# Kernel tuning notes

Measured on AMD Instinct MI355X. Metric: run time of the kernel, lower is better.

Reference implementation:

```python
import jax, jax.numpy as jnp
import numpy as np

B, N, E = 2, 2048, 1024
H, D = 16, 64  # context_dim = H*D = 1024


def setup_inputs() -> dict:
    key = jax.random.key(0)
    ks = jax.random.split(key, 6)
    s = 0.02
    return {
        "input_emb": jax.random.normal(ks[0], (B, N, E), dtype=jnp.float32),
        "Wq": jax.random.normal(ks[1], (E, H * D), dtype=jnp.float32) * s,
        "Wk": jax.random.normal(ks[2], (E, D), dtype=jnp.float32) * s,
        "Wv": jax.random.normal(ks[3], (E, D), dtype=jnp.float32) * s,
        "Wo": jax.random.normal(ks[4], (H * D, H * D), dtype=jnp.float32) * s,
        "bo": jax.random.normal(ks[5], (H * D,), dtype=jnp.float32) * s,
    }


def reference(input_emb, Wq, Wk, Wv, Wo, bo):
    b, n, _ = input_emb.shape
    Q = (input_emb @ Wq).reshape(b, n, H, D)          # (B,N,H,D)
    K = input_emb @ Wk                                 # (B,N,D) shared across heads (MQA)
    V = input_emb @ Wv                                 # (B,N,D)
    # scores: (B,H,N,N); mask is applied before scaling in the torch code,
    # but -inf/scale == -inf so mask-then-scale == scale-then-mask.
    scores = jnp.einsum("bnhd,bmd->bhnm", Q, K) / jnp.sqrt(jnp.float32(D))
    causal = jnp.tril(jnp.ones((n, n), dtype=bool))    # True = keep
    scores = jnp.where(causal[None, None], scores, -jnp.inf)
    weights = jax.nn.softmax(scores, axis=-1)          # dropout rate 0.0 -> identity
    Z = jnp.einsum("bhnm,bmd->bnhd", weights, V).reshape(b, n, H * D)
    return Z @ Wo + bo
```

## Files before the change

### kernel.cpp

```cpp
#include <hip/hip_runtime.h>
#include <hip/hip_bf16.h>


#define NQ 2048
#define BATCH 2
#define HEADS 16
#define HD 64
#define EMB 1024
#define NKV 1152

typedef short s16x8 __attribute__((ext_vector_type(8)));
typedef float f32x4 __attribute__((ext_vector_type(4)));
typedef unsigned short ushort_t;

__device__ __forceinline__ ushort_t f2bf(float f) {
    unsigned u = __builtin_bit_cast(unsigned, f);
    u += 0x7fff + ((u >> 16) & 1);
    return (ushort_t)(u >> 16);
}

__device__ __forceinline__ void store_out(float* p, float v) { *p = v; }
__device__ __forceinline__ void store_out(ushort_t* p, float v) { *p = f2bf(v); }

#define GL16(g, l)                                                                  \
    __builtin_amdgcn_global_load_lds(                                               \
        (const __attribute__((address_space(1))) unsigned int*)(g),                 \
        (__attribute__((address_space(3))) unsigned int*)(l), 16, 0, 0)

__global__ __launch_bounds__(256) void prep(const float* __restrict__ x,
                                            const float* __restrict__ Wq,
                                            const float* __restrict__ Wk,
                                            const float* __restrict__ Wv,
                                            const float* __restrict__ Wo,
                                            ushort_t* __restrict__ xb,
                                            ushort_t* __restrict__ Wqkv_t,
                                            ushort_t* __restrict__ Wo_t) {
    const int bid = blockIdx.x, t = threadIdx.x;
    if (bid < 4096) {
        const int i = bid * 1024 + t * 4;
        const float4 v = *(const float4*)&x[i];
        ushort_t o[4] = {f2bf(v.x), f2bf(v.y), f2bf(v.z), f2bf(v.w)};
        *(uint2*)&xb[i] = *(uint2*)o;
        return;
    }
    int tb = bid - 4096;
    const float* src; ushort_t* dst; int N, n0, k0;
    if (tb < 1024)      { src = Wq; N = 1024; dst = Wqkv_t;
                          n0 = (tb & 31) * 32; k0 = (tb >> 5) * 32; }
    else if (tb < 1088) { tb -= 1024; src = Wk; N = 64; dst = Wqkv_t + (size_t)1024 * EMB;
                          n0 = (tb & 1) * 32; k0 = (tb >> 1) * 32; }
    else if (tb < 1152) { tb -= 1088; src = Wv; N = 64; dst = Wqkv_t + (size_t)1088 * EMB;
                          n0 = (tb & 1) * 32; k0 = (tb >> 1) * 32; }
    else                { tb -= 1152; src = Wo; N = 1024; dst = Wo_t;
                          n0 = (tb & 31) * 32; k0 = (tb >> 5) * 32; }
    __shared__ float tile[32][33];
    const int tx = t & 31, ty = t >> 5;
#pragma unroll
    for (int i = 0; i < 32; i += 8)
        tile[ty + i][tx] = src[(size_t)(k0 + ty + i) * N + n0 + tx];
    __syncthreads();
#pragma unroll
    for (int i = 0; i < 32; i += 8)
        dst[(size_t)(n0 + ty + i) * EMB + k0 + tx] = f2bf(tile[tx][ty + i]);
}

template<bool HAS_BIAS, bool WRITE_VT, typename OutT>
__global__ __launch_bounds__(256) void gemm_bf16(const ushort_t* __restrict__ A,
                                                 const ushort_t* __restrict__ Bt,
                                                 const float* __restrict__ bias,
                                                 OutT* __restrict__ C,
                                                 ushort_t* __restrict__ Vt,
                                                 int M, int N, int K) {
    __shared__ __align__(16) ushort_t Al[64 * 32];
    __shared__ __align__(16) ushort_t Bl[128 * 32];
    const int t = threadIdx.x;
    const int w = t >> 6, lane = t & 63, quad = lane >> 4, ln = lane & 15;
    const int row0 = blockIdx.y * 64, col0 = blockIdx.x * 128;

    const int rA = t >> 2;
    const int lcA = (t & 3) ^ ((rA >> 1) & 3);
    const int rB1 = 64 + rA;
    const ushort_t* ga  = A  + (size_t)(row0 + rA) * K + lcA * 8;
    const ushort_t* gb0 = Bt + (size_t)(col0 + rA) * K + lcA * 8;
    const ushort_t* gb1 = Bt + (size_t)(col0 + rB1) * K + lcA * 8;
    ushort_t* lA  = Al + w * 512;
    ushort_t* lB0 = Bl + w * 512;
    ushort_t* lB1 = Bl + 2048 + w * 512;

    f32x4 acc[4][2] = {};
    const int sw = (ln >> 1) & 3;
    for (int k0 = 0; k0 < K; k0 += 32) {
        GL16(ga, lA); GL16(gb0, lB0); GL16(gb1, lB1);
        ga += 32; gb0 += 32; gb1 += 32;
        __syncthreads();

        s16x8 af[4], bf[2];
#pragma unroll
        for (int mt = 0; mt < 4; ++mt)
            af[mt] = *(const s16x8*)&Al[(mt * 16 + ln) * 32 + ((quad ^ sw) * 8)];
#pragma unroll
        for (int nt = 0; nt < 2; ++nt)
            bf[nt] = *(const s16x8*)&Bl[(w * 32 + nt * 16 + ln) * 32 + ((quad ^ sw) * 8)];
#pragma unroll
        for (int mt = 0; mt < 4; ++mt)
#pragma unroll
            for (int nt = 0; nt < 2; ++nt)
                acc[mt][nt] = __builtin_amdgcn_mfma_f32_16x16x32_bf16(
                    af[mt], bf[nt], acc[mt][nt], 0, 0, 0);
        __syncthreads();
    }

#pragma unroll
    for (int nt = 0; nt < 2; ++nt) {
        const int col = col0 + w * 32 + nt * 16 + ln;
        const float bv = HAS_BIAS ? bias[col] : 0.f;
#pragma unroll
        for (int mt = 0; mt < 4; ++mt) {
#pragma unroll
            for (int r = 0; r < 4; ++r) {
                const int row = row0 + mt * 16 + quad * 4 + r;
                store_out(&C[(size_t)row * N + col], acc[mt][nt][r] + bv);
            }
            if (WRITE_VT && col >= 1088) {
                const int d = col - 1088;
                const int n = row0 + mt * 16 + quad * 4;
                const int bb = n >> 11, nn = n & 2047;
                ushort_t tmp[4] = {f2bf(acc[mt][nt][0]), f2bf(acc[mt][nt][1]),
                                   f2bf(acc[mt][nt][2]), f2bf(acc[mt][nt][3])};
                *(uint2*)&Vt[((size_t)bb * 64 + d) * NQ + nn] = *(uint2*)tmp;
            }
        }
    }
}

__device__ __forceinline__ void stage_tile(ushort_t* lds, const ushort_t* g,
                                           size_t rstride, int w, int lane) {
#pragma unroll
    for (int it = 0; it < 2; ++it) {
        const int u = (w * 2 + it) * 64 + lane;
        const int row = u >> 3, pc = u & 7;
        const int lc = pc ^ (row & 7);
        GL16(g + (size_t)row * rstride + lc * 8, lds + (size_t)(w * 2 + it) * 512);
    }
}

__device__ __forceinline__ s16x8 frag(const ushort_t* lds, int row, int lc) {
    const int phys = lc ^ (row & 7);
    return *(const s16x8*)&lds[row * 64 + phys * 8];
}

__global__ __launch_bounds__(256, 4) void attn_mfma(const ushort_t* __restrict__ QKV,
                                                    const ushort_t* __restrict__ Vt,
                                                    ushort_t* __restrict__ Z) {
    const int bid = blockIdx.x;
    const int b = (bid >> 4) & 1, h = bid & 15;
    const int i = bid >> 5, k = i >> 3, j = i & 7;
    const int qt = (k == 0) ? 2 * j : (k == 1) ? 31 - 2 * j
                 : (k == 2) ? 2 * j + 1 : 30 - 2 * j;
    const int t = threadIdx.x;
    const int w = t >> 6, lane = t & 63, quad = lane >> 4, ln = lane & 15;

    __shared__ __align__(16) ushort_t QPs[64 * 64];
    __shared__ __align__(16) ushort_t Kl[2][64 * 64];
    __shared__ __align__(16) ushort_t Vl[2][64 * 64];

    const ushort_t* Kg = QKV + (size_t)b * NQ * NKV + 1024;
    const ushort_t* Vg = Vt + (size_t)b * 64 * NQ;

    stage_tile(QPs, QKV + (size_t)(b * NQ + qt * 64) * NKV + h * HD, NKV, w, lane);
    stage_tile(Kl[0], Kg, NKV, w, lane);
    stage_tile(Vl[0], Vg, NQ, w, lane);
    __syncthreads();

    const s16x8 aQ0 = frag(QPs, w * 16 + ln, quad);
    const s16x8 aQ1 = frag(QPs, w * 16 + ln, 4 + quad);

    f32x4 o[4];
#pragma unroll
    for (int ii = 0; ii < 4; ++ii) o[ii] = f32x4{0.f, 0.f, 0.f, 0.f};
    float mrow[4], lrow[4];
#pragma unroll
    for (int r = 0; r < 4; ++r) { mrow[r] = -1e30f; lrow[r] = 0.f; }

#pragma unroll 1
    for (int jt = 0; jt <= qt; ++jt) {
        const int cur = jt & 1;
        if (jt < qt) {
            stage_tile(Kl[cur ^ 1], Kg + (size_t)(jt + 1) * 64 * NKV, NKV, w, lane);
            stage_tile(Vl[cur ^ 1], Vg + (jt + 1) * 64, NQ, w, lane);
        }
        const ushort_t* Kc = Kl[cur];
        const ushort_t* Vc = Vl[cur];

        f32x4 s[4];
#pragma unroll
        for (int nt = 0; nt < 4; ++nt) {
            f32x4 acc = f32x4{0.f, 0.f, 0.f, 0.f};
            const s16x8 b0 = frag(Kc, nt * 16 + ln, quad);
            const s16x8 b1 = frag(Kc, nt * 16 + ln, 4 + quad);
            acc = __builtin_amdgcn_mfma_f32_16x16x32_bf16(aQ0, b0, acc, 0, 0, 0);
            acc = __builtin_amdgcn_mfma_f32_16x16x32_bf16(aQ1, b1, acc, 0, 0, 0);
            s[nt] = acc;
        }

        const bool diag = (jt == qt);
        float rmax[4];
#pragma unroll
        for (int r = 0; r < 4; ++r) rmax[r] = -1e30f;
#pragma unroll
        for (int nt = 0; nt < 4; ++nt)
#pragma unroll
            for (int r = 0; r < 4; ++r) {
                float v = s[nt][r] * 0.125f;
                if (diag && (nt * 16 + ln) > (w * 16 + quad * 4 + r)) v = -1e30f;
                s[nt][r] = v;
                rmax[r] = fmaxf(rmax[r], v);
            }
#pragma unroll
        for (int r = 0; r < 4; ++r) {
            rmax[r] = fmaxf(rmax[r], __shfl_xor(rmax[r], 1));
            rmax[r] = fmaxf(rmax[r], __shfl_xor(rmax[r], 2));
            rmax[r] = fmaxf(rmax[r], __shfl_xor(rmax[r], 4));
            rmax[r] = fmaxf(rmax[r], __shfl_xor(rmax[r], 8));
        }
        float alpha[4], rsum[4];
#pragma unroll
        for (int r = 0; r < 4; ++r) {
            const float mnew = fmaxf(mrow[r], rmax[r]);
            alpha[r] = __expf(mrow[r] - mnew);
            mrow[r] = mnew;
            rsum[r] = 0.f;
        }
#pragma unroll
        for (int nt = 0; nt < 4; ++nt)
#pragma unroll
            for (int r = 0; r < 4; ++r) {
                const float pv = __expf(s[nt][r] - mrow[r]);
                s[nt][r] = pv;
                rsum[r] += pv;
            }
#pragma unroll
        for (int r = 0; r < 4; ++r) {
            rsum[r] += __shfl_xor(rsum[r], 1);
            rsum[r] += __shfl_xor(rsum[r], 2);
            rsum[r] += __shfl_xor(rsum[r], 4);
            rsum[r] += __shfl_xor(rsum[r], 8);
            lrow[r] = lrow[r] * alpha[r] + rsum[r];
        }
#pragma unroll
        for (int ntd = 0; ntd < 4; ++ntd)
#pragma unroll
            for (int r = 0; r < 4; ++r) o[ntd][r] *= alpha[r];

#pragma unroll
        for (int nt = 0; nt < 4; ++nt)
#pragma unroll
            for (int r = 0; r < 4; ++r) {
                const int prow = quad * 4 + r;
                const int pc = (nt * 2 + (ln >> 3)) ^ (prow & 7);
                QPs[(w * 16 + prow) * 64 + pc * 8 + (ln & 7)] = f2bf(s[nt][r]);
            }
        asm volatile("s_waitcnt lgkmcnt(0)" ::: "memory");

        const s16x8 aP0 = frag(QPs, w * 16 + ln, quad);
        const s16x8 aP1 = frag(QPs, w * 16 + ln, 4 + quad);
#pragma unroll
        for (int ntd = 0; ntd < 4; ++ntd) {
            const s16x8 b0 = frag(Vc, ntd * 16 + ln, quad);
            const s16x8 b1 = frag(Vc, ntd * 16 + ln, 4 + quad);
            o[ntd] = __builtin_amdgcn_mfma_f32_16x16x32_bf16(aP0, b0, o[ntd], 0, 0, 0);
            o[ntd] = __builtin_amdgcn_mfma_f32_16x16x32_bf16(aP1, b1, o[ntd], 0, 0, 0);
        }
        __syncthreads();
    }

    float invl[4];
#pragma unroll
    for (int r = 0; r < 4; ++r) invl[r] = 1.f / lrow[r];
#pragma unroll
    for (int ntd = 0; ntd < 4; ++ntd)
#pragma unroll
        for (int r = 0; r < 4; ++r) {
            const size_t row = (size_t)(b * NQ + qt * 64 + w * 16 + quad * 4 + r);
            Z[row * EMB + h * HD + ntd * 16 + ln] = f2bf(o[ntd][r] * invl[r]);
        }
}

extern "C" void kernel_launch(void* const* d_in, const int* in_sizes, int n_in,
                              void* d_out, int out_size, void* d_ws, size_t ws_size,
                              hipStream_t stream) {
    const float* x  = (const float*)d_in[0];
    const float* Wq = (const float*)d_in[1];
    const float* Wk = (const float*)d_in[2];
    const float* Wv = (const float*)d_in[3];
    const float* Wo = (const float*)d_in[4];
    const float* bo = (const float*)d_in[5];
    float* out = (float*)d_out;

    const int M = BATCH * NQ;
    char* ws = (char*)d_ws;
    ushort_t* xb     = (ushort_t*)ws;
    ushort_t* Wqkv_t = (ushort_t*)(ws + (size_t)8  * 1024 * 1024);
    ushort_t* Wo_t   = (ushort_t*)(ws + (size_t)11 * 1024 * 1024);
    ushort_t* QKV    = (ushort_t*)(ws + (size_t)13 * 1024 * 1024);
    ushort_t* Vt     = (ushort_t*)(ws + (size_t)23 * 1024 * 1024);
    ushort_t* Zb     = (ushort_t*)(ws + (size_t)24 * 1024 * 1024);

    dim3 blk(256);
    prep<<<dim3(6272), blk, 0, stream>>>(x, Wq, Wk, Wv, Wo, xb, Wqkv_t, Wo_t);
    gemm_bf16<false, true, ushort_t><<<dim3(NKV / 128, M / 64), blk, 0, stream>>>(
        xb, Wqkv_t, nullptr, QKV, Vt, M, NKV, EMB);
    attn_mfma<<<dim3(1024), blk, 0, stream>>>(QKV, Vt, Zb);
    gemm_bf16<true, false, float><<<dim3(EMB / 128, M / 64), blk, 0, stream>>>(
        Zb, Wo_t, bo, out, nullptr, M, EMB, EMB);
}
```

Baseline: 188.5 us.

## Transpose attention MFMA layout to keep P in registers, fold scale into Q

The QK^T MFMA now takes K as the A operand, so each lane holds one query row. K rows are permuted during staging so the score fragment can be packed straight into the B operand of the PV MFMA with v_cvt_pk_bf16_f32, removing the LDS round trip for P and the Q staging buffer. The softmax scale and log2(e) are folded into Q in the projection GEMM epilogue so exp2 can be used, and rescaling of the running max is skipped when the max grows by at most 8. It also adds s_setprio around the MFMA blocks and vectorizes the Z stores, at the cost of tricky index permutations that must stay consistent.

```diff
diff --git a/kernel.cpp b/kernel.cpp
--- a/kernel.cpp
+++ b/kernel.cpp
@@ -11,6 +11,7 @@
 
 typedef short s16x8 __attribute__((ext_vector_type(8)));
 typedef float f32x4 __attribute__((ext_vector_type(4)));
+typedef unsigned int u32x4 __attribute__((ext_vector_type(4)));
 typedef unsigned short ushort_t;
 
 __device__ __forceinline__ ushort_t f2bf(float f) {
@@ -119,7 +120,9 @@
 #pragma unroll
             for (int r = 0; r < 4; ++r) {
                 const int row = row0 + mt * 16 + quad * 4 + r;
-                store_out(&C[(size_t)row * N + col], acc[mt][nt][r] + bv);
+                float v = acc[mt][nt][r] + bv;
+                if (WRITE_VT && col < 1024) v *= 0.18033688011112043f;
+                store_out(&C[(size_t)row * N + col], v);
             }
             if (WRITE_VT && col >= 1088) {
                 const int d = col - 1088;
@@ -141,6 +144,19 @@
         const int row = u >> 3, pc = u & 7;
         const int lc = pc ^ (row & 7);
         GL16(g + (size_t)row * rstride + lc * 8, lds + (size_t)(w * 2 + it) * 512);
+    }
+}
+
+__device__ __forceinline__ void stage_k(ushort_t* lds, const ushort_t* g,
+                                        int w, int lane) {
+#pragma unroll
+    for (int it = 0; it < 2; ++it) {
+        const int u = (w * 2 + it) * 64 + lane;
+        const int row = u >> 3, pc = u & 7;
+        const int lc = pc ^ (row & 7);
+        const int grow = (row & 32) | (((row >> 2) & 3) << 3) |
+                         (((row >> 4) & 1) << 2) | (row & 3);
+        GL16(g + (size_t)grow * NKV + lc * 8, lds + (size_t)(w * 2 + it) * 512);
     }
 }
 
@@ -160,130 +176,126 @@
     const int t = threadIdx.x;
     const int w = t >> 6, lane = t & 63, quad = lane >> 4, ln = lane & 15;
 
-    __shared__ __align__(16) ushort_t QPs[64 * 64];
     __shared__ __align__(16) ushort_t Kl[2][64 * 64];
     __shared__ __align__(16) ushort_t Vl[2][64 * 64];
 
     const ushort_t* Kg = QKV + (size_t)b * NQ * NKV + 1024;
     const ushort_t* Vg = Vt + (size_t)b * 64 * NQ;
 
-    stage_tile(QPs, QKV + (size_t)(b * NQ + qt * 64) * NKV + h * HD, NKV, w, lane);
-    stage_tile(Kl[0], Kg, NKV, w, lane);
+    const ushort_t* Qg = QKV + (size_t)(b * NQ + qt * 64 + w * 16 + ln) * NKV + h * HD;
+    const s16x8 aQ0 = *(const s16x8*)(Qg + quad * 8);
+    const s16x8 aQ1 = *(const s16x8*)(Qg + 32 + quad * 8);
+
+    stage_k(Kl[0], Kg, w, lane);
     stage_tile(Vl[0], Vg, NQ, w, lane);
     __syncthreads();
 
-    const s16x8 aQ0 = frag(QPs, w * 16 + ln, quad);
-    const s16x8 aQ1 = frag(QPs, w * 16 + ln, 4 + quad);
-
     f32x4 o[4];
 #pragma unroll
     for (int ii = 0; ii < 4; ++ii) o[ii] = f32x4{0.f, 0.f, 0.f, 0.f};
-    float mrow[4], lrow[4];
-#pragma unroll
-    for (int r = 0; r < 4; ++r) { mrow[r] = -1e30f; lrow[r] = 0.f; }
+    float mrow = -1e30f, lrow = 0.f;
+    const int qrel = w * 16 + ln;
 
 #pragma unroll 1
     for (int jt = 0; jt <= qt; ++jt) {
         const int cur = jt & 1;
         if (jt < qt) {
-            stage_tile(Kl[cur ^ 1], Kg + (size_t)(jt + 1) * 64 * NKV, NKV, w, lane);
+            stage_k(Kl[cur ^ 1], Kg + (size_t)(jt + 1) * 64 * NKV, w, lane);
             stage_tile(Vl[cur ^ 1], Vg + (jt + 1) * 64, NQ, w, lane);
         }
         const ushort_t* Kc = Kl[cur];
         const ushort_t* Vc = Vl[cur];
 
         f32x4 s[4];
+        __builtin_amdgcn_s_setprio(1);
 #pragma unroll
         for (int nt = 0; nt < 4; ++nt) {
             f32x4 acc = f32x4{0.f, 0.f, 0.f, 0.f};
-            const s16x8 b0 = frag(Kc, nt * 16 + ln, quad);
-            const s16x8 b1 = frag(Kc, nt * 16 + ln, 4 + quad);
-            acc = __builtin_amdgcn_mfma_f32_16x16x32_bf16(aQ0, b0, acc, 0, 0, 0);
-            acc = __builtin_amdgcn_mfma_f32_16x16x32_bf16(aQ1, b1, acc, 0, 0, 0);
+            acc = __builtin_amdgcn_mfma_f32_16x16x32_bf16(
+                frag(Kc, nt * 16 + ln, quad), aQ0, acc, 0, 0, 0);
+            acc = __builtin_amdgcn_mfma_f32_16x16x32_bf16(
+                frag(Kc, nt * 16 + ln, 4 + quad), aQ1, acc, 0, 0, 0);
             s[nt] = acc;
         }
-
-        const bool diag = (jt == qt);
-        float rmax[4];
-#pragma unroll
-        for (int r = 0; r < 4; ++r) rmax[r] = -1e30f;
+        __builtin_amdgcn_s_setprio(0);
+
+        if (jt == qt) {
+#pragma unroll
+            for (int nt = 0; nt < 4; ++nt)
+#pragma unroll
+                for (int r = 0; r < 4; ++r) {
+                    const int kv = (nt >> 1) * 32 + quad * 8 + (nt & 1) * 4 + r;
+                    if (kv > qrel) s[nt][r] = -1e30f;
+                }
+        }
+
+        float m0 = fmaxf(fmaxf(s[0][0], s[0][1]), fmaxf(s[0][2], s[0][3]));
+        float m1 = fmaxf(fmaxf(s[1][0], s[1][1]), fmaxf(s[1][2], s[1][3]));
+        float m2 = fmaxf(fmaxf(s[2][0], s[2][1]), fmaxf(s[2][2], s[2][3]));
+        float m3 = fmaxf(fmaxf(s[3][0], s[3][1]), fmaxf(s[3][2], s[3][3]));
+        float rmax = fmaxf(fmaxf(m0, m1), fmaxf(m2, m3));
+        rmax = fmaxf(rmax, __shfl_xor(rmax, 16));
+        rmax = fmaxf(rmax, __shfl_xor(rmax, 32));
+
+        if (!__all(rmax - mrow <= 8.f)) {
+            const float mnew = fmaxf(mrow, rmax);
+            const float al = __builtin_amdgcn_exp2f(mrow - mnew);
+            mrow = mnew;
+            lrow *= al;
+#pragma unroll
+            for (int ntd = 0; ntd < 4; ++ntd)
+#pragma unroll
+                for (int r = 0; r < 4; ++r) o[ntd][r] *= al;
+        }
+
+        float rsum = 0.f;
 #pragma unroll
         for (int nt = 0; nt < 4; ++nt)
 #pragma unroll
             for (int r = 0; r < 4; ++r) {
-                float v = s[nt][r] * 0.125f;
-                if (diag && (nt * 16 + ln) > (w * 16 + quad * 4 + r)) v = -1e30f;
-                s[nt][r] = v;
-                rmax[r] = fmaxf(rmax[r], v);
+                const float pv = __builtin_amdgcn_exp2f(s[nt][r] - mrow);
+                s[nt][r] = pv;
+                rsum += pv;
             }
-#pragma unroll
-        for (int r = 0; r < 4; ++r) {
-            rmax[r] = fmaxf(rmax[r], __shfl_xor(rmax[r], 1));
-            rmax[r] = fmaxf(rmax[r], __shfl_xor(rmax[r], 2));
-            rmax[r] = fmaxf(rmax[r], __shfl_xor(rmax[r], 4));
-            rmax[r] = fmaxf(rmax[r], __shfl_xor(rmax[r], 8));
-        }
-        float alpha[4], rsum[4];
-#pragma unroll
-        for (int r = 0; r < 4; ++r) {
-            const float mnew = fmaxf(mrow[r], rmax[r]);
-            alpha[r] = __expf(mrow[r] - mnew);
-            mrow[r] = mnew;
-            rsum[r] = 0.f;
-        }
-#pragma unroll
-        for (int nt = 0; nt < 4; ++nt)
-#pragma unroll
-            for (int r = 0; r < 4; ++r) {
-                const float pv = __expf(s[nt][r] - mrow[r]);
-                s[nt][r] = pv;
-                rsum[r] += pv;
-            }
-#pragma unroll
-        for (int r = 0; r < 4; ++r) {
-            rsum[r] += __shfl_xor(rsum[r], 1);
-            rsum[r] += __shfl_xor(rsum[r], 2);
-            rsum[r] += __shfl_xor(rsum[r], 4);
-            rsum[r] += __shfl_xor(rsum[r], 8);
-            lrow[r] = lrow[r] * alpha[r] + rsum[r];
-        }
-#pragma unroll
-        for (int ntd = 0; ntd < 4; ++ntd)
-#pragma unroll
-            for (int r = 0; r < 4; ++r) o[ntd][r] *= alpha[r];
-
-#pragma unroll
-        for (int nt = 0; nt < 4; ++nt)
-#pragma unroll
-            for (int r = 0; r < 4; ++r) {
-                const int prow = quad * 4 + r;
-                const int pc = (nt * 2 + (ln >> 3)) ^ (prow & 7);
-                QPs[(w * 16 + prow) * 64 + pc * 8 + (ln & 7)] = f2bf(s[nt][r]);
-            }
-        asm volatile("s_waitcnt lgkmcnt(0)" ::: "memory");
-
-        const s16x8 aP0 = frag(QPs, w * 16 + ln, quad);
-        const s16x8 aP1 = frag(QPs, w * 16 + ln, 4 + quad);
+        rsum += __shfl_xor(rsum, 16);
+        rsum += __shfl_xor(rsum, 32);
+        lrow += rsum;
+
+        unsigned pw0[4], pw1[4];
+#pragma unroll
+        for (int jj = 0; jj < 4; ++jj) {
+            const int nt0 = jj >> 1, rr = 2 * (jj & 1);
+            asm("v_cvt_pk_bf16_f32 %0, %1, %2"
+                : "=v"(pw0[jj]) : "v"(s[nt0][rr]), "v"(s[nt0][rr + 1]));
+            asm("v_cvt_pk_bf16_f32 %0, %1, %2"
+                : "=v"(pw1[jj]) : "v"(s[2 + nt0][rr]), "v"(s[2 + nt0][rr + 1]));
+        }
+        const u32x4 q0 = {pw0[0], pw0[1], pw0[2], pw0[3]};
+        const u32x4 q1 = {pw1[0], pw1[1], pw1[2], pw1[3]};
+        const s16x8 bP0 = __builtin_bit_cast(s16x8, q0);
+        const s16x8 bP1 = __builtin_bit_cast(s16x8, q1);
+
+        __builtin_amdgcn_s_setprio(1);
 #pragma unroll
         for (int ntd = 0; ntd < 4; ++ntd) {
-            const s16x8 b0 = frag(Vc, ntd * 16 + ln, quad);
-            const s16x8 b1 = frag(Vc, ntd * 16 + ln, 4 + quad);
-            o[ntd] = __builtin_amdgcn_mfma_f32_16x16x32_bf16(aP0, b0, o[ntd], 0, 0, 0);
-            o[ntd] = __builtin_amdgcn_mfma_f32_16x16x32_bf16(aP1, b1, o[ntd], 0, 0, 0);
-        }
+            o[ntd] = __builtin_amdgcn_mfma_f32_16x16x32_bf16(
+                frag(Vc, ntd * 16 + ln, quad), bP0, o[ntd], 0, 0, 0);
+            o[ntd] = __builtin_amdgcn_mfma_f32_16x16x32_bf16(
+                frag(Vc, ntd * 16 + ln, 4 + quad), bP1, o[ntd], 0, 0, 0);
+        }
+        __builtin_amdgcn_s_setprio(0);
         __syncthreads();
     }
 
-    float invl[4];
-#pragma unroll
-    for (int r = 0; r < 4; ++r) invl[r] = 1.f / lrow[r];
-#pragma unroll
-    for (int ntd = 0; ntd < 4; ++ntd)
-#pragma unroll
-        for (int r = 0; r < 4; ++r) {
-            const size_t row = (size_t)(b * NQ + qt * 64 + w * 16 + quad * 4 + r);
-            Z[row * EMB + h * HD + ntd * 16 + ln] = f2bf(o[ntd][r] * invl[r]);
-        }
+    const float invl = 1.f / lrow;
+    const size_t row = (size_t)(b * NQ + qt * 64 + w * 16 + ln);
+#pragma unroll
+    for (int ntd = 0; ntd < 4; ++ntd) {
+        ushort_t tmp[4];
+#pragma unroll
+        for (int r = 0; r < 4; ++r) tmp[r] = f2bf(o[ntd][r] * invl);
+        *(uint2*)&Z[row * EMB + h * HD + ntd * 16 + quad * 4] = *(uint2*)tmp;
+    }
 }
 
 extern "C" void kernel_launch(void* const* d_in, const int* in_sizes, int n_in,
```

Result: faster. 166.5 us (-11.7%).
